# Kernel tuning notes

Hardware: AMD Instinct MI355X
Metric: run time of the kernel (lower is better)

Reference implementation:

```python
import jax, jax.numpy as jnp
import numpy as np
from jax import lax

WIN = 9
PAD = WIN // 2  # floor(9/2) = 4, 'same' spatial output


def _box_sum(x):
    # 3D sliding-window sum via conv with a ones kernel [1,1,9,9,9]
    k = jnp.ones((1, 1, WIN, WIN, WIN), x.dtype)
    return lax.conv_general_dilated(
        x, k,
        window_strides=(1, 1, 1),
        padding=[(PAD, PAD)] * 3,
        dimension_numbers=('NCDHW', 'OIDHW', 'NCDHW'),
    )


def setup_inputs() -> dict:
    key = jax.random.key(0)
    k1, k2 = jax.random.split(key)
    shape = (2, 1, 160, 160, 160)  # [B, C=1, D, H, W] 3D volumes
    return {
        'y_true': jax.random.normal(k1, shape, dtype=jnp.float32),
        'y_pred': jax.random.normal(k2, shape, dtype=jnp.float32),
    }


def reference(y_true, y_pred):
    win_size = float(WIN ** 3)  # 729
    I, J = y_true, y_pred
    I_sum = _box_sum(I)
    J_sum = _box_sum(J)
    I2_sum = _box_sum(I * I)
    J2_sum = _box_sum(J * J)
    IJ_sum = _box_sum(I * J)
    u_I = I_sum / win_size
    u_J = J_sum / win_size
    cross = IJ_sum - u_J * I_sum - u_I * J_sum + u_I * u_J * win_size
    I_var = I2_sum - 2.0 * u_I * I_sum + u_I * u_I * win_size
    J_var = J2_sum - 2.0 * u_J * J_sum + u_J * u_J * win_size
    cc = cross * cross / (I_var * J_var + 1e-5)
    return -jnp.mean(cc)
```

## Files before the change

kernel.cpp:

```cpp
#include <hip/hip_runtime.h>


#define NB   2
#define NDIM 160
#define TILE 32
#define RE   40
#define DCHUNK 32
#define NDCHUNK (NDIM / DCHUNK)
#define NSLICE (DCHUNK + 8)
#define NBLK ((NDIM/TILE)*(NDIM/TILE)*NB*NDCHUNK)
#define NTHR 1024
#define SLICE_SZ (NDIM * NDIM)

__global__ __launch_bounds__(NTHR)
void ncc_main(const float* __restrict__ I, const float* __restrict__ J,
              double* __restrict__ out_acc, unsigned int* __restrict__ out_cnt,
              float* __restrict__ out) {
    const int t  = threadIdx.x;
    const int tx = t & 31;
    const int ty = t >> 5;
    const int w0 = blockIdx.x * TILE;
    const int h0 = blockIdx.y * TILE;
    const int b  = blockIdx.z / NDCHUNK;
    const int d0 = (blockIdx.z % NDCHUNK) * DCHUNK;

    const float* Ib = I + (size_t)b * NDIM * SLICE_SZ;
    const float* Jb = J + (size_t)b * NDIM * SLICE_SZ;

    __shared__ float  sI[2][RE][RE + 1];
    __shared__ float  sJ[2][RE][RE + 1];
    __shared__ float4 rs4[RE][TILE + 1];
    __shared__ float  rss[RE][TILE + 1];
    __shared__ double wsum[NTHR / 64];

    const int e1 = t + NTHR;
    const int r0 = t / RE,  c0 = t - r0 * RE;
    const int r1 = e1 / RE, c1 = e1 - r1 * RE;
    const int h_0 = h0 - 4 + r0, w_0 = w0 - 4 + c0;
    const int h_1 = h0 - 4 + r1, w_1 = w0 - 4 + c1;
    const bool has1 = (e1 < RE * RE);
    const bool in0 = ((unsigned)h_0 < NDIM) && ((unsigned)w_0 < NDIM);
    const bool in1 = has1 && ((unsigned)h_1 < NDIM) && ((unsigned)w_1 < NDIM);
    const int idx0 = h_0 * NDIM + w_0;
    const int idx1 = h_1 * NDIM + w_1;

    float ring[9][5];
#pragma unroll
    for (int k = 0; k < 9; ++k)
#pragma unroll
        for (int c = 0; c < 5; ++c) ring[k][c] = 0.0f;

    float acc[5] = {0.f, 0.f, 0.f, 0.f, 0.f};
    double csum = 0.0;
    const float inv_win = 1.0f / 729.0f;
    int cur = 0;

    {
        const int dz0 = d0 - 4;
        if ((unsigned)dz0 < NDIM) {
            const float* Iz = Ib + (size_t)dz0 * SLICE_SZ;
            const float* Jz = Jb + (size_t)dz0 * SLICE_SZ;
            float vi0 = in0 ? Iz[idx0] : 0.f;
            float vj0 = in0 ? Jz[idx0] : 0.f;
            sI[0][r0][c0] = vi0;
            sJ[0][r0][c0] = vj0;
            if (has1) {
                float vi1 = in1 ? Iz[idx1] : 0.f;
                float vj1 = in1 ? Jz[idx1] : 0.f;
                sI[0][r1][c1] = vi1;
                sJ[0][r1][c1] = vj1;
            }
        }
        __syncthreads();
    }

    for (int o = 0; o < 5; ++o) {
#pragma unroll
        for (int j = 0; j < 9; ++j) {
            const int step = o * 9 + j;
            const int dz = d0 - 4 + step;
            float s[5] = {0.f, 0.f, 0.f, 0.f, 0.f};
            if (step < NSLICE) {
                const int dzn = dz + 1;
                const bool pf = (step + 1 < NSLICE) && ((unsigned)dzn < NDIM);
                float pvi0 = 0.f, pvj0 = 0.f, pvi1 = 0.f, pvj1 = 0.f;
                if (pf) {
                    const float* Iz = Ib + (size_t)dzn * SLICE_SZ;
                    const float* Jz = Jb + (size_t)dzn * SLICE_SZ;
                    if (in0) { pvi0 = Iz[idx0]; pvj0 = Jz[idx0]; }
                    if (in1) { pvi1 = Iz[idx1]; pvj1 = Jz[idx1]; }
                }
                if ((unsigned)dz < NDIM) {
                    for (int p = t; p < RE * TILE; p += NTHR) {
                        int r = p >> 5, wo = p & 31;
                        float a0 = 0.f, a1 = 0.f, a2 = 0.f, a3 = 0.f, a4 = 0.f;
#pragma unroll
                        for (int k = 0; k < 9; ++k) {
                            float vi = sI[cur][r][wo + k];
                            float vj = sJ[cur][r][wo + k];
                            a0 += vi; a1 += vj;
                            a2 += vi * vi; a3 += vj * vj; a4 += vi * vj;
                        }
                        rs4[r][wo] = make_float4(a0, a1, a2, a3);
                        rss[r][wo] = a4;
                    }
                }
                if (pf) {
                    const int nxt = cur ^ 1;
                    sI[nxt][r0][c0] = pvi0;
                    sJ[nxt][r0][c0] = pvj0;
                    if (has1) {
                        sI[nxt][r1][c1] = pvi1;
                        sJ[nxt][r1][c1] = pvj1;
                    }
                }
                __syncthreads();
                if ((unsigned)dz < NDIM) {
                    float s0 = 0.f, s1 = 0.f, s2 = 0.f, s3 = 0.f, s4 = 0.f;
#pragma unroll
                    for (int k = 0; k < 9; ++k) {
                        float4 v = rs4[ty + k][tx];
                        s0 += v.x; s1 += v.y; s2 += v.z; s3 += v.w;
                        s4 += rss[ty + k][tx];
                    }
                    s[0] = s0; s[1] = s1; s[2] = s2; s[3] = s3; s[4] = s4;
                }
                __syncthreads();
                cur ^= 1;
            }
#pragma unroll
            for (int c = 0; c < 5; ++c) {
                acc[c] += s[c] - ring[j][c];
                ring[j][c] = s[c];
            }
            if (step >= 8 && step < 8 + DCHUNK) {
                float Is = acc[0], Js = acc[1];
                float I2 = acc[2], J2 = acc[3], IJ = acc[4];
                float cross = IJ - Is * Js * inv_win;
                float Ivar  = I2 - Is * Is * inv_win;
                float Jvar  = J2 - Js * Js * inv_win;
                float cc = cross * cross / (Ivar * Jvar + 1e-5f);
                csum += (double)cc;
            }
        }
    }

#pragma unroll
    for (int off = 32; off > 0; off >>= 1)
        csum += __shfl_down(csum, off, 64);
    if ((t & 63) == 0) wsum[t >> 6] = csum;
    __syncthreads();
    if (t == 0) {
        double total = 0.0;
#pragma unroll
        for (int wv = 0; wv < NTHR / 64; ++wv) total += wsum[wv];
        atomicAdd(out_acc, total);
        __threadfence();
        unsigned int old = atomicAdd(out_cnt, 1u);
        if (old == NBLK - 1) {
            double fin = atomicAdd(out_acc, 0.0);
            out[0] = (float)(-fin / 8192000.0);
        }
    }
}

extern "C" void kernel_launch(void* const* d_in, const int* in_sizes, int n_in,
                              void* d_out, int out_size, void* d_ws, size_t ws_size,
                              hipStream_t stream) {
    const float* I = (const float*)d_in[0];
    const float* J = (const float*)d_in[1];
    double* acc = (double*)d_ws;
    unsigned int* cnt = (unsigned int*)((char*)d_ws + 8);

    hipMemsetAsync(d_ws, 0, 16, stream);

    dim3 grid(NDIM / TILE, NDIM / TILE, NB * NDCHUNK);
    ncc_main<<<grid, NTHR, 0, stream>>>(I, J, acc, cnt, (float*)d_out);
}
```

Before: 146.4 us.

## Shrink tiles to 16x32 with 512 threads and interleave I/J in shared memory

Halves the tile width to 16 with a 24-wide halo and drops the block to 512 threads, doubling the number of blocks. This is meant to improve occupancy and load balance across CUs. I and J are now stored as float2 in one shared array, so each tap needs one wider LDS read instead of two. The cost is a larger halo fraction: a 24-wide halo for 16 outputs versus 40 for 32 means more redundant global loads and more horizontal-pass work per output.

```diff
diff --git a/kernel.cpp b/kernel.cpp
--- a/kernel.cpp
+++ b/kernel.cpp
@@ -3,13 +3,16 @@
 
 #define NB   2
 #define NDIM 160
-#define TILE 32
-#define RE   40
+#define TW   16
+#define TH   32
+#define REW  24
+#define REH  40
+#define NPTS (REH * REW)
 #define DCHUNK 32
 #define NDCHUNK (NDIM / DCHUNK)
 #define NSLICE (DCHUNK + 8)
-#define NBLK ((NDIM/TILE)*(NDIM/TILE)*NB*NDCHUNK)
-#define NTHR 1024
+#define NBLK ((NDIM/TW)*(NDIM/TH)*NB*NDCHUNK)
+#define NTHR 512
 #define SLICE_SZ (NDIM * NDIM)
 
 __global__ __launch_bounds__(NTHR)
@@ -17,28 +20,27 @@
               double* __restrict__ out_acc, unsigned int* __restrict__ out_cnt,
               float* __restrict__ out) {
     const int t  = threadIdx.x;
-    const int tx = t & 31;
-    const int ty = t >> 5;
-    const int w0 = blockIdx.x * TILE;
-    const int h0 = blockIdx.y * TILE;
+    const int tx = t & 15;
+    const int ty = t >> 4;
+    const int w0 = blockIdx.x * TW;
+    const int h0 = blockIdx.y * TH;
     const int b  = blockIdx.z / NDCHUNK;
     const int d0 = (blockIdx.z % NDCHUNK) * DCHUNK;
 
     const float* Ib = I + (size_t)b * NDIM * SLICE_SZ;
     const float* Jb = J + (size_t)b * NDIM * SLICE_SZ;
 
-    __shared__ float  sI[2][RE][RE + 1];
-    __shared__ float  sJ[2][RE][RE + 1];
-    __shared__ float4 rs4[RE][TILE + 1];
-    __shared__ float  rss[RE][TILE + 1];
+    __shared__ float2 sIJ[2][REH][REW + 1];
+    __shared__ float4 rs4[REH][TW + 1];
+    __shared__ float  rss[REH][TW + 1];
     __shared__ double wsum[NTHR / 64];
 
     const int e1 = t + NTHR;
-    const int r0 = t / RE,  c0 = t - r0 * RE;
-    const int r1 = e1 / RE, c1 = e1 - r1 * RE;
+    const int r0 = t / REW,  c0 = t - r0 * REW;
+    const int r1 = e1 / REW, c1 = e1 - r1 * REW;
     const int h_0 = h0 - 4 + r0, w_0 = w0 - 4 + c0;
     const int h_1 = h0 - 4 + r1, w_1 = w0 - 4 + c1;
-    const bool has1 = (e1 < RE * RE);
+    const bool has1 = (e1 < NPTS);
     const bool in0 = ((unsigned)h_0 < NDIM) && ((unsigned)w_0 < NDIM);
     const bool in1 = has1 && ((unsigned)h_1 < NDIM) && ((unsigned)w_1 < NDIM);
     const int idx0 = h_0 * NDIM + w_0;
@@ -62,13 +64,11 @@
             const float* Jz = Jb + (size_t)dz0 * SLICE_SZ;
             float vi0 = in0 ? Iz[idx0] : 0.f;
             float vj0 = in0 ? Jz[idx0] : 0.f;
-            sI[0][r0][c0] = vi0;
-            sJ[0][r0][c0] = vj0;
+            sIJ[0][r0][c0] = make_float2(vi0, vj0);
             if (has1) {
                 float vi1 = in1 ? Iz[idx1] : 0.f;
                 float vj1 = in1 ? Jz[idx1] : 0.f;
-                sI[0][r1][c1] = vi1;
-                sJ[0][r1][c1] = vj1;
+                sIJ[0][r1][c1] = make_float2(vi1, vj1);
             }
         }
         __syncthreads();
@@ -91,15 +91,14 @@
                     if (in1) { pvi1 = Iz[idx1]; pvj1 = Jz[idx1]; }
                 }
                 if ((unsigned)dz < NDIM) {
-                    for (int p = t; p < RE * TILE; p += NTHR) {
-                        int r = p >> 5, wo = p & 31;
+                    for (int p = t; p < REH * TW; p += NTHR) {
+                        int r = p >> 4, wo = p & 15;
                         float a0 = 0.f, a1 = 0.f, a2 = 0.f, a3 = 0.f, a4 = 0.f;
 #pragma unroll
                         for (int k = 0; k < 9; ++k) {
-                            float vi = sI[cur][r][wo + k];
-                            float vj = sJ[cur][r][wo + k];
-                            a0 += vi; a1 += vj;
-                            a2 += vi * vi; a3 += vj * vj; a4 += vi * vj;
+                            float2 v = sIJ[cur][r][wo + k];
+                            a0 += v.x; a1 += v.y;
+                            a2 += v.x * v.x; a3 += v.y * v.y; a4 += v.x * v.y;
                         }
                         rs4[r][wo] = make_float4(a0, a1, a2, a3);
                         rss[r][wo] = a4;
@@ -107,12 +106,8 @@
                 }
                 if (pf) {
                     const int nxt = cur ^ 1;
-                    sI[nxt][r0][c0] = pvi0;
-                    sJ[nxt][r0][c0] = pvj0;
-                    if (has1) {
-                        sI[nxt][r1][c1] = pvi1;
-                        sJ[nxt][r1][c1] = pvj1;
-                    }
+                    sIJ[nxt][r0][c0] = make_float2(pvi0, pvj0);
+                    if (has1) sIJ[nxt][r1][c1] = make_float2(pvi1, pvj1);
                 }
                 __syncthreads();
                 if ((unsigned)dz < NDIM) {
@@ -174,6 +169,6 @@
 
     hipMemsetAsync(d_ws, 0, 16, stream);
 
-    dim3 grid(NDIM / TILE, NDIM / TILE, NB * NDCHUNK);
+    dim3 grid(NDIM / TW, NDIM / TH, NB * NDCHUNK);
     ncc_main<<<grid, NTHR, 0, stream>>>(I, J, acc, cnt, (float*)d_out);
 }
```

Result: slower. 180.6 us (+23.3%).
